# Optimization experiments

Measured on AMD Instinct MI355X. Metric: run time of the kernel, lower is better.

## Reference

```python
import jax, jax.numpy as jnp
import numpy as np

H = 16
D_MODEL = 1024
HEAD_DIM = D_MODEL // H
NEG = -1e9


def setup_inputs() -> dict:
    key = jax.random.key(0)
    k1, k2, k3, k4, k5, k6 = jax.random.split(key, 6)
    B, L = 2, 2048
    feature = jax.random.normal(k1, (B, L, D_MODEL), dtype=jnp.float32)
    mask = jax.random.randint(k2, (B, L), 0, 2, dtype=jnp.int32)
    # Linear weights stored torch-style as [out, in]; biases zero-init per initialize().
    s = 1.0 / np.sqrt(D_MODEL)
    W_Q = jax.random.uniform(k3, (D_MODEL, D_MODEL), jnp.float32, -s, s)
    W_K = jax.random.uniform(k4, (D_MODEL, D_MODEL), jnp.float32, -s, s)
    W_V = jax.random.uniform(k5, (D_MODEL, D_MODEL), jnp.float32, -s, s)
    b_Q = jnp.zeros((D_MODEL,), jnp.float32)
    b_K = jnp.zeros((D_MODEL,), jnp.float32)
    b_V = jnp.zeros((D_MODEL,), jnp.float32)
    return {"feature": feature, "mask": mask, "W_Q": W_Q, "b_Q": b_Q,
            "W_K": W_K, "b_K": b_K, "W_V": W_V, "b_V": b_V}


def reference(feature, mask, W_Q, b_Q, W_K, b_K, W_V, b_V):
    B, L, _ = feature.shape
    scale = jnp.sqrt(jnp.float32(HEAD_DIM))
    # Projections: torch Linear is x @ W^T + b. Split into heads: [B, H, L, Dh]
    def proj(W, b):
        y = feature @ W.T + b
        return y.reshape(B, L, H, HEAD_DIM).transpose(0, 2, 1, 3)
    Q = proj(W_Q, b_Q)
    K = proj(W_K, b_K)
    V = proj(W_V, b_V)
    # Scores [B, H, Lq, Lk]
    A = jnp.einsum('bhqd,bhkd->bhqk', Q, K) / scale
    # Key-side mask broadcast over heads and query positions
    A = jnp.where(mask[:, None, None, :] == 0, jnp.float32(NEG), A)
    alpha = jax.nn.softmax(A, axis=-1)
    out = jnp.einsum('bhqk,bhkd->bhqd', alpha, V)  # [B, H, L, Dh]
    return out.transpose(0, 2, 1, 3).reshape(B, L, H * HEAD_DIM)
```

## Files before the change

kernel.cpp:

```cpp
#include <hip/hip_runtime.h>

typedef __bf16 bf16;
typedef __attribute__((ext_vector_type(4))) __bf16 bf16x4;
typedef __attribute__((ext_vector_type(8))) __bf16 bf16x8;
typedef __attribute__((ext_vector_type(4))) float f32x4;
typedef __attribute__((ext_vector_type(16))) float f32x16;
typedef unsigned int u32;

#define D_MODEL 1024
#define SEQ_L   2048
#define NHEAD   16
#define HDIM    64
#define MROWS   4096

#define S_SCALE 0.18033688f

#define FEAT_OFF  512u
#define WQ_OFF    (FEAT_OFF + 4194304u)
#define WK_OFF    (WQ_OFF + 1048576u)
#define WV_OFF    (WK_OFF + 1048576u)
#define BQ_OFF    (WV_OFF + 1048576u)
#define BK_OFF    (BQ_OFF + 1024u)
#define BV_OFF    (BK_OFF + 1024u)
#define Q_OFF     (BV_OFF + 1024u)
#define K_OFF     (Q_OFF + 4194304u)
#define V_OFF     (K_OFF + 4194304u)

typedef const __attribute__((address_space(1))) u32* gp_t;
typedef __attribute__((address_space(3))) u32* lp_t;
__device__ __forceinline__ void ld16(const bf16* g, bf16* l) {
    __builtin_amdgcn_global_load_lds((gp_t)g, (lp_t)l, 16, 0, 0);
}

__global__ void convert_in(const float* __restrict__ feat,
                           const float* __restrict__ wq, const float* __restrict__ wk,
                           const float* __restrict__ wv,
                           const float* __restrict__ bq, const float* __restrict__ bk,
                           const float* __restrict__ bv,
                           bf16* __restrict__ ws) {
    const int bid = blockIdx.x;
    const float* src; bf16* dst; int off; float sc = 1.0f;
    if (bid < 4096)      { src = feat; dst = ws + FEAT_OFF; off = bid * 1024; }
    else if (bid < 5120) { src = wq;   dst = ws + WQ_OFF;   off = (bid - 4096) * 1024; sc = S_SCALE; }
    else if (bid < 6144) { src = wk;   dst = ws + WK_OFF;   off = (bid - 5120) * 1024; }
    else if (bid < 7168) { src = wv;   dst = ws + WV_OFF;   off = (bid - 6144) * 1024; }
    else if (bid == 7168){ src = bq;   dst = ws + BQ_OFF;   off = 0; sc = S_SCALE; }
    else if (bid == 7169){ src = bk;   dst = ws + BK_OFF;   off = 0; }
    else                 { src = bv;   dst = ws + BV_OFF;   off = 0; }
    int idx = off + threadIdx.x * 4;
    float4 v = *(const float4*)(src + idx);
    dst[idx + 0] = (bf16)(v.x * sc);
    dst[idx + 1] = (bf16)(v.y * sc);
    dst[idx + 2] = (bf16)(v.z * sc);
    dst[idx + 3] = (bf16)(v.w * sc);
}

__global__ __launch_bounds__(256, 2) void qkv_gemm(const bf16* __restrict__ ws,
                                                   bf16* __restrict__ wsw,
                                                   const int* __restrict__ mask) {
    const int zi = blockIdx.z;
    const bf16* Amat = (zi == 2) ? ws + WV_OFF : ws + FEAT_OFF;
    const bf16* Bmat = (zi == 0) ? ws + WQ_OFF : (zi == 1) ? ws + WK_OFF : ws + FEAT_OFF;
    const bf16* bias = ws + ((zi == 0) ? BQ_OFF : (zi == 1) ? BK_OFF : BV_OFF);
    bf16* Y = (zi == 2) ? wsw + V_OFF : wsw + Q_OFF + (size_t)zi * 4194304u;

    __shared__ bf16 Alds[128 * 64];
    __shared__ bf16 Blds[128 * 64];

    const int t    = threadIdx.x;
    const int lane = t & 63;
    const int wave = t >> 6;
    const int quad = lane >> 4;
    const int l16  = lane & 15;
    const int m0   = ((zi == 2) ? blockIdx.y : blockIdx.x) * 128;
    const int n0   = ((zi == 2) ? blockIdx.x : blockIdx.y) * 128;
    const int wrow = (wave >> 1) * 64;
    const int wcol = (wave & 1) * 64;

    const int r8 = lane >> 3;
    const int sl = lane & 7;
    const int sg = sl ^ r8;

    f32x4 acc[4][4];
    for (int mi = 0; mi < 4; ++mi)
        for (int ni = 0; ni < 4; ++ni)
            acc[mi][ni] = (f32x4){0.f, 0.f, 0.f, 0.f};

    for (int k0 = 0; k0 < D_MODEL; k0 += 64) {
#pragma unroll
        for (int i = 0; i < 4; ++i) {
            int ch  = wave * 4 + i;
            int row = ch * 8 + r8;
            ld16(Amat + (size_t)(m0 + row) * D_MODEL + k0 + sg * 8, Alds + ch * 512);
            ld16(Bmat + (size_t)(n0 + row) * D_MODEL + k0 + sg * 8, Blds + ch * 512);
        }
        __syncthreads();

#pragma unroll
        for (int kk = 0; kk < 2; ++kk) {
            const int sgb = quad + kk * 4;
            bf16x8 af[4], bfr[4];
#pragma unroll
            for (int mi = 0; mi < 4; ++mi) {
                int row = wrow + mi * 16 + l16;
                af[mi] = *(const bf16x8*)(&Alds[row * 64 + ((sgb ^ (row & 7)) << 3)]);
            }
#pragma unroll
            for (int ni = 0; ni < 4; ++ni) {
                int row = wcol + ni * 16 + l16;
                bfr[ni] = *(const bf16x8*)(&Blds[row * 64 + ((sgb ^ (row & 7)) << 3)]);
            }
#pragma unroll
            for (int mi = 0; mi < 4; ++mi)
#pragma unroll
                for (int ni = 0; ni < 4; ++ni)
                    acc[mi][ni] = __builtin_amdgcn_mfma_f32_16x16x32_bf16(
                        af[mi], bfr[ni], acc[mi][ni], 0, 0, 0);
        }
        __syncthreads();
    }

    if (zi < 2) {
#pragma unroll
        for (int ni = 0; ni < 4; ++ni) {
            int col = n0 + wcol + ni * 16 + l16;
            float bvf = (float)bias[col];
#pragma unroll
            for (int mi = 0; mi < 4; ++mi) {
                int rowb = m0 + wrow + mi * 16 + quad * 4;
#pragma unroll
                for (int r = 0; r < 4; ++r) {
                    float v = acc[mi][ni][r] + bvf;
                    if (zi == 1 && mask[rowb + r] == 0) v = 0.f;
                    Y[(size_t)(rowb + r) * D_MODEL + col] = (bf16)v;
                }
            }
        }
    } else {
#pragma unroll
        for (int mi = 0; mi < 4; ++mi) {
#pragma unroll
            for (int r = 0; r < 4; ++r) {
                int rowv = m0 + wrow + mi * 16 + quad * 4 + r;
                float bvf = (float)bias[rowv];
#pragma unroll
                for (int ni = 0; ni < 4; ++ni) {
                    int col = n0 + wcol + ni * 16 + l16;
                    float v = acc[mi][ni][r] + bvf;
                    if (mask[col] == 0) v = 0.f;
                    size_t addr = (size_t)(col >> 11) * 2097152u +
                                  (size_t)rowv * 2048u + (col & 2047);
                    Y[addr] = (bf16)v;
                }
            }
        }
    }
}

__global__ __launch_bounds__(128, 4) void attn_kernel(
    const bf16* __restrict__ ws, bf16* __restrict__ wsw,
    const int* __restrict__ mask, float* __restrict__ out) {
    const int bh  = blockIdx.x;
    const int qt  = blockIdx.y;
    const int ks2 = blockIdx.z;
    const int b   = bh >> 4, h = bh & 15;
    const int t    = threadIdx.x;
    const int lane = t & 63;
    const int wave = t >> 6;
    const int half = lane >> 5;
    const int l31  = lane & 31;
    const int kt0  = ks2 * 1024;

    __shared__ bf16 Klds[64 * 64];
    __shared__ bf16 Vlds[64 * 64];

    const bf16* Qh  = ws + Q_OFF + (size_t)(b * SEQ_L) * D_MODEL + h * HDIM;
    const bf16* Kh  = ws + K_OFF + (size_t)(b * SEQ_L) * D_MODEL + h * HDIM;
    const bf16* Vth = ws + V_OFF + (size_t)b * 2097152u + (size_t)(h * HDIM) * SEQ_L;

    const int qrow0 = qt * 64 + wave * 32;
    bf16x8 qf[4];
#pragma unroll
    for (int ks = 0; ks < 4; ++ks)
        qf[ks] = *(const bf16x8*)(Qh + (size_t)(qrow0 + l31) * D_MODEL
                                  + ks * 16 + half * 8);

    bf16x8 ones;
#pragma unroll
    for (int j = 0; j < 8; ++j) ones[j] = (bf16)1.0f;

    f32x16 o[2], lacc;
    int nm = 0;
#pragma unroll
    for (int i = 0; i < 16; ++i) { o[0][i] = 0.f; o[1][i] = 0.f; lacc[i] = 0.f; }

    const int srow = (lane >> 3);
    const int sg   = (lane & 7) ^ srow;

    for (int kt = kt0; kt < kt0 + 1024; kt += 64) {
#pragma unroll
        for (int i = 0; i < 4; ++i) {
            int row = i * 16 + wave * 8 + srow;
            ld16(Kh + (size_t)(kt + row) * D_MODEL + sg * 8,
                 Klds + i * 1024 + wave * 512);
            ld16(Vth + (size_t)row * SEQ_L + kt + sg * 8,
                 Vlds + i * 1024 + wave * 512);
        }
        int mv = mask[b * SEQ_L + kt + lane];
        nm += (int)__popcll(__ballot(mv != 0));
        __syncthreads();

        f32x16 st[2];
#pragma unroll
        for (int ktile = 0; ktile < 2; ++ktile) {
#pragma unroll
            for (int i = 0; i < 16; ++i) st[ktile][i] = 0.f;
#pragma unroll
            for (int ks = 0; ks < 4; ++ks) {
                const int row  = ktile * 32 + l31;
                const int slot = (ks * 2 + half) ^ (l31 & 7);
                bf16x8 kf = *(const bf16x8*)(&Klds[row * 64 + slot * 8]);
                st[ktile] = __builtin_amdgcn_mfma_f32_32x32x16_bf16(
                    kf, qf[ks], st[ktile], 0, 0, 0);
            }
        }

        bf16x4 pk[2][4];
#pragma unroll
        for (int ktile = 0; ktile < 2; ++ktile) {
#pragma unroll
            for (int g = 0; g < 4; ++g) {
                bf16x4 pkv;
#pragma unroll
                for (int j = 0; j < 4; ++j)
                    pkv[j] = (bf16)__builtin_amdgcn_exp2f(st[ktile][g * 4 + j]);
                pk[ktile][g] = pkv;
            }
        }

        bf16x8 pf[4];
#pragma unroll
        for (int ks = 0; ks < 4; ++ks) {
            const int k1 = ks & 1, kt2 = ks >> 1;
            uint2 a  = __builtin_bit_cast(uint2, pk[kt2][2 * k1]);
            uint2 bb = __builtin_bit_cast(uint2, pk[kt2][2 * k1 + 1]);
            uint2 keep, send;
            keep.x = half ? bb.x : a.x;  keep.y = half ? bb.y : a.y;
            send.x = half ? a.x : bb.x;  send.y = half ? a.y : bb.y;
            uint2 recv;
            recv.x = (unsigned)__shfl_xor((int)send.x, 32);
            recv.y = (unsigned)__shfl_xor((int)send.y, 32);
            uint4 frag;
            frag.x = half ? recv.x : keep.x;
            frag.y = half ? recv.y : keep.y;
            frag.z = half ? keep.x : recv.x;
            frag.w = half ? keep.y : recv.y;
            pf[ks] = __builtin_bit_cast(bf16x8, frag);
        }

#pragma unroll
        for (int ks = 0; ks < 4; ++ks)
            lacc = __builtin_amdgcn_mfma_f32_32x32x16_bf16(pf[ks], ones, lacc, 0, 0, 0);
#pragma unroll
        for (int dt = 0; dt < 2; ++dt) {
#pragma unroll
            for (int ks = 0; ks < 4; ++ks) {
                const int row  = dt * 32 + l31;
                const int slot = (ks * 2 + half) ^ (l31 & 7);
                bf16x8 vf = *(const bf16x8*)(&Vlds[row * 64 + slot * 8]);
                o[dt] = __builtin_amdgcn_mfma_f32_32x32x16_bf16(
                    pf[ks], vf, o[dt], 0, 0, 0);
            }
        }
        __syncthreads();
    }

    float* Lp  = (float*)(wsw + WQ_OFF);
    bf16*  O1  = wsw + FEAT_OFF;
    const float corr = (float)(1024 - nm);
#pragma unroll
    for (int r = 0; r < 16; ++r) {
        const int q32 = (r & 3) + 8 * (r >> 2) + 4 * half;
        const int q = qrow0 + q32;
        const size_t base = ((size_t)(b * SEQ_L + q)) * D_MODEL + h * HDIM;
        if (l31 == 0)
            Lp[ks2 * 65536 + bh * 2048 + qrow0 + q32] = lacc[r] - corr;
        if (ks2 == 0) {
            out[base + l31]      = o[0][r];
            out[base + 32 + l31] = o[1][r];
        } else {
            O1[base + l31]      = (bf16)o[0][r];
            O1[base + 32 + l31] = (bf16)o[1][r];
        }
    }
}

__global__ void combine(float* __restrict__ out, const bf16* __restrict__ ws) {
    const float* Lp = (const float*)(ws + WQ_OFF);
    const bf16*  O1 = ws + FEAT_OFF;
    int idx = (blockIdx.x * 256 + threadIdx.x) * 4;
    int row = idx >> 10;
    int col = idx & 1023;
    int b = row >> 11, q = row & 2047, h = col >> 6;
    int li = (b * 16 + h) * 2048 + q;
    float rl = 1.0f / fmaxf(Lp[li] + Lp[65536 + li], 1e-30f);
    float4 o0 = *(float4*)(out + idx);
    bf16x4 o1 = *(const bf16x4*)(O1 + idx);
    float4 res;
    res.x = (o0.x + (float)o1[0]) * rl;
    res.y = (o0.y + (float)o1[1]) * rl;
    res.z = (o0.z + (float)o1[2]) * rl;
    res.w = (o0.w + (float)o1[3]) * rl;
    *(float4*)(out + idx) = res;
}

extern "C" void kernel_launch(void* const* d_in, const int* in_sizes, int n_in,
                              void* d_out, int out_size, void* d_ws, size_t ws_size,
                              hipStream_t stream) {
    const float* feat = (const float*)d_in[0];
    const int*   mask = (const int*)d_in[1];
    const float* Wq = (const float*)d_in[2];
    const float* bq = (const float*)d_in[3];
    const float* Wk = (const float*)d_in[4];
    const float* bk = (const float*)d_in[5];
    const float* Wv = (const float*)d_in[6];
    const float* bv = (const float*)d_in[7];

    bf16* ws = (bf16*)d_ws;

    convert_in<<<7171, 256, 0, stream>>>(feat, Wq, Wk, Wv, bq, bk, bv, ws);

    dim3 g1(32, 8, 3);
    qkv_gemm<<<g1, 256, 0, stream>>>(ws, ws, mask);

    dim3 g2(2 * NHEAD, SEQ_L / 64, 2);
    attn_kernel<<<g2, 128, 0, stream>>>(ws, ws, mask, (float*)d_out);

    combine<<<4096, 256, 0, stream>>>((float*)d_out, ws);
}
```

Baseline: 175.7 us.

## Double-buffer K/V tiles in LDS and widen attention blocks to four waves

Each attention block now has four waves covering 128 query rows instead of two waves covering 64, so every K/V tile loaded into LDS is shared by twice as many waves. The K/V staging becomes a two-buffer ping-pong: the next tile is prefetched while the current one is consumed, and the barrier before compute is removed. The aim is to hide global-to-LDS load latency and halve redundant K/V traffic. The cost is double the LDS footprint, larger blocks and half as many blocks in the grid, which may reduce occupancy.

```diff
diff --git a/kernel.cpp b/kernel.cpp
--- a/kernel.cpp
+++ b/kernel.cpp
@@ -157,7 +157,7 @@
     }
 }
 
-__global__ __launch_bounds__(128, 4) void attn_kernel(
+__global__ __launch_bounds__(256, 4) void attn_kernel(
     const bf16* __restrict__ ws, bf16* __restrict__ wsw,
     const int* __restrict__ mask, float* __restrict__ out) {
     const int bh  = blockIdx.x;
@@ -171,14 +171,14 @@
     const int l31  = lane & 31;
     const int kt0  = ks2 * 1024;
 
-    __shared__ bf16 Klds[64 * 64];
-    __shared__ bf16 Vlds[64 * 64];
+    __shared__ bf16 Klds[2][64 * 64];
+    __shared__ bf16 Vlds[2][64 * 64];
 
     const bf16* Qh  = ws + Q_OFF + (size_t)(b * SEQ_L) * D_MODEL + h * HDIM;
     const bf16* Kh  = ws + K_OFF + (size_t)(b * SEQ_L) * D_MODEL + h * HDIM;
     const bf16* Vth = ws + V_OFF + (size_t)b * 2097152u + (size_t)(h * HDIM) * SEQ_L;
 
-    const int qrow0 = qt * 64 + wave * 32;
+    const int qrow0 = qt * 128 + wave * 32;
     bf16x8 qf[4];
 #pragma unroll
     for (int ks = 0; ks < 4; ++ks)
@@ -197,18 +197,27 @@
     const int srow = (lane >> 3);
     const int sg   = (lane & 7) ^ srow;
 
+#define STAGE(bb, kt)                                                          \
+    do {                                                                       \
+        _Pragma("unroll")                                                      \
+        for (int i = 0; i < 2; ++i) {                                          \
+            int row = i * 32 + wave * 8 + srow;                                \
+            ld16(Kh + (size_t)((kt) + row) * D_MODEL + sg * 8,                 \
+                 &Klds[bb][i * 2048 + wave * 512]);                            \
+            ld16(Vth + (size_t)row * SEQ_L + (kt) + sg * 8,                    \
+                 &Vlds[bb][i * 2048 + wave * 512]);                            \
+        }                                                                      \
+    } while (0)
+
+    STAGE(0, kt0);
+    __syncthreads();
+
+    int cur = 0;
     for (int kt = kt0; kt < kt0 + 1024; kt += 64) {
-#pragma unroll
-        for (int i = 0; i < 4; ++i) {
-            int row = i * 16 + wave * 8 + srow;
-            ld16(Kh + (size_t)(kt + row) * D_MODEL + sg * 8,
-                 Klds + i * 1024 + wave * 512);
-            ld16(Vth + (size_t)row * SEQ_L + kt + sg * 8,
-                 Vlds + i * 1024 + wave * 512);
-        }
+        if (kt + 64 < kt0 + 1024) STAGE(cur ^ 1, kt + 64);
+
         int mv = mask[b * SEQ_L + kt + lane];
         nm += (int)__popcll(__ballot(mv != 0));
-        __syncthreads();
 
         f32x16 st[2];
 #pragma unroll
@@ -219,7 +228,7 @@
             for (int ks = 0; ks < 4; ++ks) {
                 const int row  = ktile * 32 + l31;
                 const int slot = (ks * 2 + half) ^ (l31 & 7);
-                bf16x8 kf = *(const bf16x8*)(&Klds[row * 64 + slot * 8]);
+                bf16x8 kf = *(const bf16x8*)(&Klds[cur][row * 64 + slot * 8]);
                 st[ktile] = __builtin_amdgcn_mfma_f32_32x32x16_bf16(
                     kf, qf[ks], st[ktile], 0, 0, 0);
             }
@@ -267,13 +276,16 @@
             for (int ks = 0; ks < 4; ++ks) {
                 const int row  = dt * 32 + l31;
                 const int slot = (ks * 2 + half) ^ (l31 & 7);
-                bf16x8 vf = *(const bf16x8*)(&Vlds[row * 64 + slot * 8]);
+                bf16x8 vf = *(const bf16x8*)(&Vlds[cur][row * 64 + slot * 8]);
                 o[dt] = __builtin_amdgcn_mfma_f32_32x32x16_bf16(
                     pf[ks], vf, o[dt], 0, 0, 0);
             }
         }
+
         __syncthreads();
+        cur ^= 1;
     }
+#undef STAGE
 
     float* Lp  = (float*)(wsw + WQ_OFF);
     bf16*  O1  = wsw + FEAT_OFF;
@@ -333,8 +345,8 @@
     dim3 g1(32, 8, 3);
     qkv_gemm<<<g1, 256, 0, stream>>>(ws, ws, mask);
 
-    dim3 g2(2 * NHEAD, SEQ_L / 64, 2);
-    attn_kernel<<<g2, 128, 0, stream>>>(ws, ws, mask, (float*)d_out);
+    dim3 g2(2 * NHEAD, SEQ_L / 128, 2);
+    attn_kernel<<<g2, 256, 0, stream>>>(ws, ws, mask, (float*)d_out);
 
     combine<<<4096, 256, 0, stream>>>((float*)d_out, ws);
 }
```

Measured after the change: 173.6 us. Within noise of the previous version (-1.2%).

## Load K/V fragments directly from global memory in attention and drop LDS staging

Applied to the files above, without the earlier changes.

The attention kernel stops staging K and V tiles through shared memory with barriers; each wave now loads its MFMA operand fragments straight from global memory and relies on cache reuse across waves. Blocks grow to 256 threads covering 128 query rows, the row-sum of probabilities is accumulated in VALU instead of an extra MFMA against a ones vector, mask counting is hoisted out of the loop, and s_setprio brackets the MFMA sections. The convert kernel also writes bf16x4 vectors instead of scalars. This removes LDS traffic and syncs but makes every wave issue redundant, less coalesced global loads for K and the transposed V.

```diff
diff --git a/kernel.cpp b/kernel.cpp
--- a/kernel.cpp
+++ b/kernel.cpp
@@ -49,10 +49,12 @@
     else                 { src = bv;   dst = ws + BV_OFF;   off = 0; }
     int idx = off + threadIdx.x * 4;
     float4 v = *(const float4*)(src + idx);
-    dst[idx + 0] = (bf16)(v.x * sc);
-    dst[idx + 1] = (bf16)(v.y * sc);
-    dst[idx + 2] = (bf16)(v.z * sc);
-    dst[idx + 3] = (bf16)(v.w * sc);
+    bf16x4 o;
+    o[0] = (bf16)(v.x * sc);
+    o[1] = (bf16)(v.y * sc);
+    o[2] = (bf16)(v.z * sc);
+    o[3] = (bf16)(v.w * sc);
+    *(bf16x4*)(dst + idx) = o;
 }
 
 __global__ __launch_bounds__(256, 2) void qkv_gemm(const bf16* __restrict__ ws,
@@ -157,7 +159,43 @@
     }
 }
 
-__global__ __launch_bounds__(128, 4) void attn_kernel(
+__device__ __forceinline__ void softmax_pack(const f32x16* st, f32x4& ls,
+                                             bf16x8* pf, const int half) {
+    bf16x4 pk[2][4];
+#pragma unroll
+    for (int ktile = 0; ktile < 2; ++ktile)
+#pragma unroll
+        for (int g = 0; g < 4; ++g) {
+            bf16x4 pkv;
+#pragma unroll
+            for (int j = 0; j < 4; ++j) {
+                float e = __builtin_amdgcn_exp2f(st[ktile][g * 4 + j]);
+                ls[j] += e;
+                pkv[j] = (bf16)e;
+            }
+            pk[ktile][g] = pkv;
+        }
+#pragma unroll
+    for (int ks = 0; ks < 4; ++ks) {
+        const int k1 = ks & 1, kt2 = ks >> 1;
+        uint2 a  = __builtin_bit_cast(uint2, pk[kt2][2 * k1]);
+        uint2 bb = __builtin_bit_cast(uint2, pk[kt2][2 * k1 + 1]);
+        uint2 keep, send;
+        keep.x = half ? bb.x : a.x;  keep.y = half ? bb.y : a.y;
+        send.x = half ? a.x : bb.x;  send.y = half ? a.y : bb.y;
+        uint2 recv;
+        recv.x = (unsigned)__shfl_xor((int)send.x, 32);
+        recv.y = (unsigned)__shfl_xor((int)send.y, 32);
+        uint4 frag;
+        frag.x = half ? recv.x : keep.x;
+        frag.y = half ? recv.y : keep.y;
+        frag.z = half ? keep.x : recv.x;
+        frag.w = half ? keep.y : recv.y;
+        pf[ks] = __builtin_bit_cast(bf16x8, frag);
+    }
+}
+
+__global__ __launch_bounds__(256, 4) void attn_kernel(
     const bf16* __restrict__ ws, bf16* __restrict__ wsw,
     const int* __restrict__ mask, float* __restrict__ out) {
     const int bh  = blockIdx.x;
@@ -171,120 +209,83 @@
     const int l31  = lane & 31;
     const int kt0  = ks2 * 1024;
 
-    __shared__ bf16 Klds[64 * 64];
-    __shared__ bf16 Vlds[64 * 64];
-
     const bf16* Qh  = ws + Q_OFF + (size_t)(b * SEQ_L) * D_MODEL + h * HDIM;
     const bf16* Kh  = ws + K_OFF + (size_t)(b * SEQ_L) * D_MODEL + h * HDIM;
     const bf16* Vth = ws + V_OFF + (size_t)b * 2097152u + (size_t)(h * HDIM) * SEQ_L;
 
-    const int qrow0 = qt * 64 + wave * 32;
+    int nm = 0;
+    {
+        int mvv[16];
+#pragma unroll
+        for (int i = 0; i < 16; ++i)
+            mvv[i] = mask[b * SEQ_L + kt0 + i * 64 + lane];
+#pragma unroll
+        for (int i = 0; i < 16; ++i)
+            nm += (int)__popcll(__ballot(mvv[i] != 0));
+    }
+
+    const int qrow0 = qt * 128 + wave * 32;
     bf16x8 qf[4];
 #pragma unroll
     for (int ks = 0; ks < 4; ++ks)
         qf[ks] = *(const bf16x8*)(Qh + (size_t)(qrow0 + l31) * D_MODEL
                                   + ks * 16 + half * 8);
 
-    bf16x8 ones;
-#pragma unroll
-    for (int j = 0; j < 8; ++j) ones[j] = (bf16)1.0f;
-
-    f32x16 o[2], lacc;
-    int nm = 0;
-#pragma unroll
-    for (int i = 0; i < 16; ++i) { o[0][i] = 0.f; o[1][i] = 0.f; lacc[i] = 0.f; }
-
-    const int srow = (lane >> 3);
-    const int sg   = (lane & 7) ^ srow;
+    f32x16 o[2];
+    f32x4  ls = (f32x4){0.f, 0.f, 0.f, 0.f};
+#pragma unroll
+    for (int i = 0; i < 16; ++i) { o[0][i] = 0.f; o[1][i] = 0.f; }
 
     for (int kt = kt0; kt < kt0 + 1024; kt += 64) {
-#pragma unroll
-        for (int i = 0; i < 4; ++i) {
-            int row = i * 16 + wave * 8 + srow;
-            ld16(Kh + (size_t)(kt + row) * D_MODEL + sg * 8,
-                 Klds + i * 1024 + wave * 512);
-            ld16(Vth + (size_t)row * SEQ_L + kt + sg * 8,
-                 Vlds + i * 1024 + wave * 512);
-        }
-        int mv = mask[b * SEQ_L + kt + lane];
-        nm += (int)__popcll(__ballot(mv != 0));
-        __syncthreads();
-
         f32x16 st[2];
 #pragma unroll
+        for (int ktile = 0; ktile < 2; ++ktile)
+#pragma unroll
+            for (int i = 0; i < 16; ++i) st[ktile][i] = 0.f;
+        __builtin_amdgcn_s_setprio(1);
+#pragma unroll
         for (int ktile = 0; ktile < 2; ++ktile) {
 #pragma unroll
-            for (int i = 0; i < 16; ++i) st[ktile][i] = 0.f;
-#pragma unroll
             for (int ks = 0; ks < 4; ++ks) {
-                const int row  = ktile * 32 + l31;
-                const int slot = (ks * 2 + half) ^ (l31 & 7);
-                bf16x8 kf = *(const bf16x8*)(&Klds[row * 64 + slot * 8]);
+                bf16x8 kf = *(const bf16x8*)(Kh
+                    + (size_t)(kt + ktile * 32 + l31) * D_MODEL
+                    + ks * 16 + half * 8);
                 st[ktile] = __builtin_amdgcn_mfma_f32_32x32x16_bf16(
                     kf, qf[ks], st[ktile], 0, 0, 0);
             }
         }
-
-        bf16x4 pk[2][4];
-#pragma unroll
-        for (int ktile = 0; ktile < 2; ++ktile) {
-#pragma unroll
-            for (int g = 0; g < 4; ++g) {
-                bf16x4 pkv;
-#pragma unroll
-                for (int j = 0; j < 4; ++j)
-                    pkv[j] = (bf16)__builtin_amdgcn_exp2f(st[ktile][g * 4 + j]);
-                pk[ktile][g] = pkv;
-            }
-        }
+        __builtin_amdgcn_s_setprio(0);
 
         bf16x8 pf[4];
-#pragma unroll
-        for (int ks = 0; ks < 4; ++ks) {
-            const int k1 = ks & 1, kt2 = ks >> 1;
-            uint2 a  = __builtin_bit_cast(uint2, pk[kt2][2 * k1]);
-            uint2 bb = __builtin_bit_cast(uint2, pk[kt2][2 * k1 + 1]);
-            uint2 keep, send;
-            keep.x = half ? bb.x : a.x;  keep.y = half ? bb.y : a.y;
-            send.x = half ? a.x : bb.x;  send.y = half ? a.y : bb.y;
-            uint2 recv;
-            recv.x = (unsigned)__shfl_xor((int)send.x, 32);
-            recv.y = (unsigned)__shfl_xor((int)send.y, 32);
-            uint4 frag;
-            frag.x = half ? recv.x : keep.x;
-            frag.y = half ? recv.y : keep.y;
-            frag.z = half ? keep.x : recv.x;
-            frag.w = half ? keep.y : recv.y;
-            pf[ks] = __builtin_bit_cast(bf16x8, frag);
-        }
-
-#pragma unroll
-        for (int ks = 0; ks < 4; ++ks)
-            lacc = __builtin_amdgcn_mfma_f32_32x32x16_bf16(pf[ks], ones, lacc, 0, 0, 0);
+        softmax_pack(st, ls, pf, half);
+
+        __builtin_amdgcn_s_setprio(1);
 #pragma unroll
         for (int dt = 0; dt < 2; ++dt) {
 #pragma unroll
             for (int ks = 0; ks < 4; ++ks) {
-                const int row  = dt * 32 + l31;
-                const int slot = (ks * 2 + half) ^ (l31 & 7);
-                bf16x8 vf = *(const bf16x8*)(&Vlds[row * 64 + slot * 8]);
+                bf16x8 vf = *(const bf16x8*)(Vth
+                    + (size_t)(dt * 32 + l31) * SEQ_L
+                    + kt + ks * 16 + half * 8);
                 o[dt] = __builtin_amdgcn_mfma_f32_32x32x16_bf16(
                     pf[ks], vf, o[dt], 0, 0, 0);
             }
         }
-        __syncthreads();
+        __builtin_amdgcn_s_setprio(0);
     }
 
     float* Lp  = (float*)(wsw + WQ_OFF);
     bf16*  O1  = wsw + FEAT_OFF;
     const float corr = (float)(1024 - nm);
+    float lsum = ls[0] + ls[1] + ls[2] + ls[3];
+    lsum += __shfl_xor(lsum, 32);
+    if (half == 0)
+        Lp[ks2 * 65536 + bh * 2048 + qrow0 + l31] = lsum - corr;
 #pragma unroll
     for (int r = 0; r < 16; ++r) {
         const int q32 = (r & 3) + 8 * (r >> 2) + 4 * half;
         const int q = qrow0 + q32;
         const size_t base = ((size_t)(b * SEQ_L + q)) * D_MODEL + h * HDIM;
-        if (l31 == 0)
-            Lp[ks2 * 65536 + bh * 2048 + qrow0 + q32] = lacc[r] - corr;
         if (ks2 == 0) {
             out[base + l31]      = o[0][r];
             out[base + 32 + l31] = o[1][r];
@@ -333,8 +334,8 @@
     dim3 g1(32, 8, 3);
     qkv_gemm<<<g1, 256, 0, stream>>>(ws, ws, mask);
 
-    dim3 g2(2 * NHEAD, SEQ_L / 64, 2);
-    attn_kernel<<<g2, 128, 0, stream>>>(ws, ws, mask, (float*)d_out);
+    dim3 g2(2 * NHEAD, SEQ_L / 128, 2);
+    attn_kernel<<<g2, 256, 0, stream>>>(ws, ws, mask, (float*)d_out);
 
     combine<<<4096, 256, 0, stream>>>((float*)d_out, ws);
 }
```

Result: slower. 249.2 us (+41.8%).
